# Performance work log

Hardware: AMD Instinct MI355X
Metric: run time of the kernel (lower is better)

The kernel has to match this reference:

```python
import jax, jax.numpy as jnp
from jax import lax
import numpy as np

HH = WW = 128          # backbone feature map (2048px image / stride 16)
C_IN = 512
FEAT_STRIDE = 16
N_ANCHOR = 9
NMS_THRESH = 0.7
N_PRE_NMS = 6000
N_POST_NMS = 300
MIN_SIZE = 16
NEG = jnp.float32(-1e30)


def _anchor_base(base_size=16, ratios=(0.5, 1.0, 2.0), scales=(8, 16, 32)):
    py = px = base_size / 2.0
    ab = np.zeros((len(ratios) * len(scales), 4), np.float32)
    for i, r in enumerate(ratios):
        for j, s in enumerate(scales):
            h = base_size * s * np.sqrt(r)
            w = base_size * s * np.sqrt(1.0 / r)
            ab[i * len(scales) + j] = [py - h / 2, px - w / 2, py + h / 2, px + w / 2]
    return ab


def _shifted_anchors(hh, ww):
    # (y1, x1, y2, x2) anchors enumerated row-major over (y, x), anchors innermost
    ab = _anchor_base()
    sy = np.arange(0, hh * FEAT_STRIDE, FEAT_STRIDE, dtype=np.float32)
    sx = np.arange(0, ww * FEAT_STRIDE, FEAT_STRIDE, dtype=np.float32)
    sx, sy = np.meshgrid(sx, sy)
    shift = np.stack((sy.ravel(), sx.ravel(), sy.ravel(), sx.ravel()), axis=1)
    anc = (ab[None, :, :] + shift[:, None, :]).reshape(-1, 4)
    return jnp.asarray(anc)


def _conv(x, w, b):
    y = lax.conv_general_dilated(x, w, (1, 1), 'SAME',
                                 dimension_numbers=('NHWC', 'HWIO', 'NHWC'))
    return y + b


def _loc2bbox(anchor, loc):
    sh = anchor[:, 2] - anchor[:, 0]
    sw = anchor[:, 3] - anchor[:, 1]
    scy = anchor[:, 0] + 0.5 * sh
    scx = anchor[:, 1] + 0.5 * sw
    cy = loc[:, 0] * sh + scy
    cx = loc[:, 1] * sw + scx
    h = jnp.exp(loc[:, 2]) * sh
    w = jnp.exp(loc[:, 3]) * sw
    return jnp.stack([cy - 0.5 * h, cx - 0.5 * w, cy + 0.5 * h, cx + 0.5 * w], axis=1)


def _nms(boxes, scores, thresh, n_out):
    # Greedy NMS with a fixed output size; invalid slots are zeroed.
    y1, x1, y2, x2 = boxes[:, 0], boxes[:, 1], boxes[:, 2], boxes[:, 3]
    areas = (y2 - y1) * (x2 - x1)

    def step(valid, _):
        s = jnp.where(valid, scores, NEG)
        i = jnp.argmax(s)
        ok = s[i] > NEG
        iy1 = jnp.maximum(y1, y1[i]); ix1 = jnp.maximum(x1, x1[i])
        iy2 = jnp.minimum(y2, y2[i]); ix2 = jnp.minimum(x2, x2[i])
        inter = jnp.maximum(iy2 - iy1, 0.0) * jnp.maximum(ix2 - ix1, 0.0)
        iou = inter / (areas + areas[i] - inter + 1e-9)
        valid = valid & (iou <= thresh)  # picked box suppresses itself (iou=1)
        return valid, (i, ok)

    _, (idx, oks) = lax.scan(step, jnp.ones(scores.shape, bool), None, length=n_out)
    return boxes[idx] * oks[:, None].astype(boxes.dtype)


def _proposals(loc, fg_score, anchor, img_h, img_w, scale):
    dst = _loc2bbox(anchor, loc)
    dst = jnp.stack([jnp.clip(dst[:, 0], 0.0, img_h),
                     jnp.clip(dst[:, 1], 0.0, img_w),
                     jnp.clip(dst[:, 2], 0.0, img_h),
                     jnp.clip(dst[:, 3], 0.0, img_w)], axis=1)
    min_size = MIN_SIZE * scale
    hs = dst[:, 2] - dst[:, 0]
    ws = dst[:, 3] - dst[:, 1]
    keep = (hs >= min_size) & (ws >= min_size)
    sc = jnp.where(keep, fg_score, -jnp.inf)
    top_s, top_i = lax.top_k(sc, N_PRE_NMS)
    return _nms(dst[top_i], top_s, NMS_THRESH, N_POST_NMS)


def _rpn_forward(x, conv_w, conv_b, loc_w, loc_b, score_w, score_b, img_h, img_w, scale):
    n, hh, ww, _ = x.shape
    anchor = _shifted_anchors(hh, ww)                    # [hh*ww*9, 4]
    h = jax.nn.relu(_conv(x, conv_w, conv_b))            # [n, hh, ww, 512]
    rpn_loc = _conv(h, loc_w, loc_b).reshape(n, -1, 4)   # [n, hh*ww*9, 4]
    rpn_score_map = _conv(h, score_w, score_b)           # [n, hh, ww, 18]
    soft = jax.nn.softmax(rpn_score_map.reshape(n, hh, ww, N_ANCHOR, 2), axis=-1)
    rpn_fg = soft[..., 1].reshape(n, -1)                 # [n, hh*ww*9]
    rpn_score = rpn_score_map.reshape(n, -1, 2)
    roi = _proposals(rpn_loc[0], rpn_fg[0], anchor, img_h, img_w, scale)  # [300, 4]
    return rpn_loc, rpn_score, roi, anchor


def setup_inputs() -> dict:
    key = jax.random.key(0)
    ks = jax.random.split(key, 4)
    return {
        "x": jax.random.normal(ks[0], (1, HH, WW, C_IN), jnp.float32),
        "conv_w": jax.random.normal(ks[1], (3, 3, C_IN, 512), jnp.float32) * 0.02,
        "conv_b": jnp.zeros((512,), jnp.float32),
        "loc_w": jax.random.normal(ks[2], (1, 1, 512, 36), jnp.float32) * 0.02,
        "loc_b": jnp.zeros((36,), jnp.float32),
        "score_w": jax.random.normal(ks[3], (1, 1, 512, 18), jnp.float32) * 0.02,
        "score_b": jnp.zeros((18,), jnp.float32),
        "img_h": HH * FEAT_STRIDE,
        "img_w": WW * FEAT_STRIDE,
        "scale": 1,
    }


def reference(x, conv_w, conv_b, loc_w, loc_b, score_w, score_b, img_h, img_w, scale):
    return _rpn_forward(x, conv_w, conv_b, loc_w, loc_b, score_w, score_b,
                        float(img_h), float(img_w), float(scale))
```

## Files before the change

kernel.cpp:

```cpp
#include <hip/hip_runtime.h>
#include <math.h>

typedef unsigned int u32;
typedef unsigned long long u64;
typedef _Float16 half8 __attribute__((ext_vector_type(8)));
typedef float f32x4 __attribute__((ext_vector_type(4)));

#define N_PIX 16384
#define N_ANC 147456
#define N_PRE 6000
#define TIE_BASE 6144
#define TIE_CAP  16384

#define OFF_H      0ULL
#define OFF_BOXES  33554432ULL
#define OFF_KEYS   35913728ULL
#define OFF_W54    36503552ULL
#define OFF_B54    36634624ULL
#define OFF_HIST1  36634880ULL
#define OFF_HIST2  36897024ULL
#define OFF_CTRL   37159168ULL
#define OFF_CAND   37159424ULL
#define OFF_SBOX   37339648ULL
#define OFF_MASK   37437952ULL
#define BASE_NEEDED 41961984ULL
#define OFF_XH     41961984ULL
#define OFF_XL     58739200ULL
#define OFF_WHT    75516416ULL
#define OFF_WLT    80235008ULL
#define FULL_NEEDED 84953600ULL

#define KEY_NEGINF 0x007FFFFFu

struct AB { float v[36]; };


__global__ void k_init(u32* hist1, u32* hist2, u32* ctrl, float* roi,
                       float* w54, float* b54,
                       const float* __restrict__ loc_w, const float* __restrict__ loc_b,
                       const float* __restrict__ score_w, const float* __restrict__ score_b) {
  int i = blockIdx.x * blockDim.x + threadIdx.x;
  const int stride = gridDim.x * blockDim.x;
  const int TOT = 65536 * 2 + 64 + 1200 + 32768 + 64;
  for (; i < TOT; i += stride) {
    if (i < 65536) hist1[i] = 0u;
    else if (i < 131072) hist2[i - 65536] = 0u;
    else if (i < 131136) ctrl[i - 131072] = 0u;
    else if (i < 132336) roi[i - 131136] = 0.f;
    else if (i < 165104) {
      int j = i - 132336;
      int k = j >> 6, oc = j & 63;
      float v = 0.f;
      if (oc < 36) v = loc_w[k * 36 + oc];
      else if (oc < 54) v = score_w[k * 18 + oc - 36];
      w54[(((k >> 2) << 6) + oc) * 4 + (k & 3)] = v;
    } else {
      int oc = i - 165104;
      float v = 0.f;
      if (oc < 36) v = loc_b[oc];
      else if (oc < 54) v = score_b[oc - 36];
      b54[oc] = v;
    }
  }
}

__global__ __launch_bounds__(256) void k_split_x(const float* __restrict__ x,
                                                 _Float16* __restrict__ xh,
                                                 _Float16* __restrict__ xl) {
  const int gid = blockIdx.x * blockDim.x + threadIdx.x;
  const int base = gid << 3;
  float a[8];
  *(float4*)&a[0] = *(const float4*)(x + base);
  *(float4*)&a[4] = *(const float4*)(x + base + 4);
  half8 hh, ll;
#pragma unroll
  for (int j = 0; j < 8; ++j) {
    _Float16 hi = (_Float16)a[j];
    hh[j] = hi;
    ll[j] = (_Float16)((a[j] - (float)hi) * 2048.0f);
  }
  *(half8*)(xh + base) = hh;
  *(half8*)(xl + base) = ll;
}

__global__ __launch_bounds__(256) void k_split_w(const float* __restrict__ w,
                                                 _Float16* __restrict__ whT,
                                                 _Float16* __restrict__ wlT) {
  __shared__ _Float16 th[64][72];
  __shared__ _Float16 tl[64][72];
  const int kb = blockIdx.x;
  const int cb = blockIdx.y;
  const int t  = threadIdx.x;
  {
    const int r = t >> 2, cq = t & 3;
    float a[16];
    const float* wp = w + ((size_t)(kb * 64 + r) << 9) + cb * 64 + cq * 16;
#pragma unroll
    for (int j = 0; j < 4; ++j) *(float4*)&a[j << 2] = *(const float4*)(wp + (j << 2));
    half8 h0, h1, l0, l1;
#pragma unroll
    for (int j = 0; j < 8; ++j) {
      _Float16 hi = (_Float16)a[j];
      h0[j] = hi; l0[j] = (_Float16)((a[j] - (float)hi) * 2048.0f);
    }
#pragma unroll
    for (int j = 0; j < 8; ++j) {
      _Float16 hi = (_Float16)a[8 + j];
      h1[j] = hi; l1[j] = (_Float16)((a[8 + j] - (float)hi) * 2048.0f);
    }
    *(half8*)&th[r][cq * 16]     = h0;
    *(half8*)&th[r][cq * 16 + 8] = h1;
    *(half8*)&tl[r][cq * 16]     = l0;
    *(half8*)&tl[r][cq * 16 + 8] = l1;
  }
  __syncthreads();
  {
    const int c = t >> 2, kq = t & 3;
    half8 o0, o1, p0, p1;
#pragma unroll
    for (int j = 0; j < 8; ++j) { o0[j] = th[kq * 16 + j][c];     p0[j] = tl[kq * 16 + j][c]; }
#pragma unroll
    for (int j = 0; j < 8; ++j) { o1[j] = th[kq * 16 + 8 + j][c]; p1[j] = tl[kq * 16 + 8 + j][c]; }
    const size_t dst = (size_t)(cb * 64 + c) * 4608 + kb * 64 + kq * 16;
    *(half8*)(whT + dst)     = o0;
    *(half8*)(whT + dst + 8) = o1;
    *(half8*)(wlT + dst)     = p0;
    *(half8*)(wlT + dst + 8) = p1;
  }
}

__global__ __launch_bounds__(256, 2) void k_conv_pre(const _Float16* __restrict__ xh,
                                                     const _Float16* __restrict__ xl,
                                                     const _Float16* __restrict__ whT,
                                                     const _Float16* __restrict__ wlT,
                                                     const float* __restrict__ bias,
                                                     float* __restrict__ h) {
  __shared__ _Float16 As[2][2][4][128][8];
  __shared__ _Float16 Bs[2][2][4][128][8];

  const int y  = blockIdx.x;
  const int nb = blockIdx.y;
  const int t  = threadIdx.x;
  const int wv = t >> 6, lane = t & 63;
  const int m0 = (wv >> 1) << 6;
  const int n0 = (wv & 1) << 6;
  const int fm = lane & 15;
  const int fq = lane >> 4;

  const int s_m = t >> 1;
  const int kq0 = (t & 1) << 1;
  const int ch0 = kq0 << 3;

  f32x4 acc_hh[4][4];
  f32x4 acc_x[4][4];
#pragma unroll
  for (int i = 0; i < 4; ++i)
#pragma unroll
    for (int j = 0; j < 4; ++j) { acc_hh[i][j] = (f32x4)0.f; acc_x[i][j] = (f32x4)0.f; }

  half8 rah0, rah1, ral0, ral1, rbh0, rbh1, rbl0, rbl1;

#define CONV_LOAD(KB)                                                            \
  {                                                                              \
    const int tap_  = (KB) >> 4;                                                 \
    const int ky_   = tap_ / 3, kx_ = tap_ - ky_ * 3;                            \
    const int cin0_ = ((KB) & 15) << 5;                                          \
    const int yy_ = y + ky_ - 1;                                                 \
    const int xx_ = s_m + kx_ - 1;                                               \
    if (yy_ >= 0 && yy_ < 128 && xx_ >= 0 && xx_ < 128) {                        \
      const size_t aoff_ = (((size_t)((yy_ << 7) + xx_)) << 9) + cin0_ + ch0;    \
      rah0 = *(const half8*)(xh + aoff_);                                        \
      rah1 = *(const half8*)(xh + aoff_ + 8);                                    \
      ral0 = *(const half8*)(xl + aoff_);                                        \
      ral1 = *(const half8*)(xl + aoff_ + 8);                                    \
    } else {                                                                     \
      rah0 = (half8)(_Float16)0; rah1 = (half8)(_Float16)0;                      \
      ral0 = (half8)(_Float16)0; ral1 = (half8)(_Float16)0;                      \
    }                                                                            \
    const size_t boff_ = (size_t)(nb * 128 + s_m) * 4608 + tap_ * 512 + cin0_ + ch0; \
    rbh0 = *(const half8*)(whT + boff_);                                         \
    rbh1 = *(const half8*)(whT + boff_ + 8);                                     \
    rbl0 = *(const half8*)(wlT + boff_);                                         \
    rbl1 = *(const half8*)(wlT + boff_ + 8);                                     \
  }

#define CONV_STORE(BUF)                                                          \
  {                                                                              \
    *(half8*)As[BUF][0][kq0][s_m]     = rah0;                                    \
    *(half8*)As[BUF][0][kq0 + 1][s_m] = rah1;                                    \
    *(half8*)As[BUF][1][kq0][s_m]     = ral0;                                    \
    *(half8*)As[BUF][1][kq0 + 1][s_m] = ral1;                                    \
    *(half8*)Bs[BUF][0][kq0][s_m]     = rbh0;                                    \
    *(half8*)Bs[BUF][0][kq0 + 1][s_m] = rbh1;                                    \
    *(half8*)Bs[BUF][1][kq0][s_m]     = rbl0;                                    \
    *(half8*)Bs[BUF][1][kq0 + 1][s_m] = rbl1;                                    \
  }

  CONV_LOAD(0);
  CONV_STORE(0);
  __syncthreads();

  int cur = 0;
#pragma unroll 1
  for (int kb = 0; kb < 143; ++kb) {
    half8 ah[4], al[4], bh[4], bl[4];
#pragma unroll
    for (int i = 0; i < 4; ++i) {
      ah[i] = *(const half8*)As[cur][0][fq][m0 + (i << 4) + fm];
      al[i] = *(const half8*)As[cur][1][fq][m0 + (i << 4) + fm];
      bh[i] = *(const half8*)Bs[cur][0][fq][n0 + (i << 4) + fm];
      bl[i] = *(const half8*)Bs[cur][1][fq][n0 + (i << 4) + fm];
    }
    CONV_LOAD(kb + 1);
    __builtin_amdgcn_sched_barrier(0);
    __builtin_amdgcn_s_setprio(1);
#pragma unroll
    for (int mi = 0; mi < 4; ++mi)
#pragma unroll
      for (int ni = 0; ni < 4; ++ni) {
        acc_hh[mi][ni] = __builtin_amdgcn_mfma_f32_16x16x32_f16(ah[mi], bh[ni], acc_hh[mi][ni], 0, 0, 0);
        acc_x[mi][ni]  = __builtin_amdgcn_mfma_f32_16x16x32_f16(ah[mi], bl[ni], acc_x[mi][ni], 0, 0, 0);
        acc_x[mi][ni]  = __builtin_amdgcn_mfma_f32_16x16x32_f16(al[mi], bh[ni], acc_x[mi][ni], 0, 0, 0);
      }
    __builtin_amdgcn_s_setprio(0);
    CONV_STORE(cur ^ 1);
    __syncthreads();
    cur ^= 1;
  }
  {
    half8 ah[4], al[4], bh[4], bl[4];
#pragma unroll
    for (int i = 0; i < 4; ++i) {
      ah[i] = *(const half8*)As[cur][0][fq][m0 + (i << 4) + fm];
      al[i] = *(const half8*)As[cur][1][fq][m0 + (i << 4) + fm];
      bh[i] = *(const half8*)Bs[cur][0][fq][n0 + (i << 4) + fm];
      bl[i] = *(const half8*)Bs[cur][1][fq][n0 + (i << 4) + fm];
    }
#pragma unroll
    for (int mi = 0; mi < 4; ++mi)
#pragma unroll
      for (int ni = 0; ni < 4; ++ni) {
        acc_hh[mi][ni] = __builtin_amdgcn_mfma_f32_16x16x32_f16(ah[mi], bh[ni], acc_hh[mi][ni], 0, 0, 0);
        acc_x[mi][ni]  = __builtin_amdgcn_mfma_f32_16x16x32_f16(ah[mi], bl[ni], acc_x[mi][ni], 0, 0, 0);
        acc_x[mi][ni]  = __builtin_amdgcn_mfma_f32_16x16x32_f16(al[mi], bh[ni], acc_x[mi][ni], 0, 0, 0);
      }
  }
#undef CONV_LOAD
#undef CONV_STORE

  const float inv2048 = 1.0f / 2048.0f;
#pragma unroll
  for (int mi = 0; mi < 4; ++mi)
#pragma unroll
    for (int ni = 0; ni < 4; ++ni) {
      const int col = n0 + (ni << 4) + fm;
      const float bb = bias[(nb << 7) + col];
#pragma unroll
      for (int r = 0; r < 4; ++r) {
        const int row = m0 + (mi << 4) + (fq << 2) + r;
        float v = acc_hh[mi][ni][r] + acc_x[mi][ni][r] * inv2048 + bb;
        h[(((size_t)((y << 7) + row)) << 9) + (nb << 7) + col] = fmaxf(v, 0.f);
      }
    }
}

#define APAD 40
__global__ __launch_bounds__(256, 2) void k_conv_fb(const float* __restrict__ x,
                                                    const float* __restrict__ w,
                                                    const float* __restrict__ bias,
                                                    float* __restrict__ h) {
  __shared__ _Float16 Ah[128][APAD];
  __shared__ _Float16 Al[128][APAD];
  __shared__ _Float16 Bh[128][APAD];
  __shared__ _Float16 Bl[128][APAD];

  const int y  = blockIdx.x;
  const int nb = blockIdx.y;
  const int t  = threadIdx.x;
  const int wv = t >> 6, lane = t & 63;
  const int m0 = (wv >> 1) << 6;
  const int n0 = (wv & 1) << 6;
  const int fm = lane & 15;
  const int fq = lane >> 4;
  const int sa_m = t >> 1;
  const int sa_h = (t & 1) << 4;
  const int sb_n = t & 127;
  const int sb_kg = (t >> 7) << 4;

  f32x4 acc_hh[4][4];
  f32x4 acc_x[4][4];
#pragma unroll
  for (int i = 0; i < 4; ++i)
#pragma unroll
    for (int j = 0; j < 4; ++j) { acc_hh[i][j] = (f32x4)0.f; acc_x[i][j] = (f32x4)0.f; }

#pragma unroll 1
  for (int kb = 0; kb < 144; ++kb) {
    const int tap  = kb >> 4;
    const int ky   = tap / 3, kx = tap - ky * 3;
    const int cin0 = (kb & 15) << 5;
    {
      const int yy = y + ky - 1;
      const int xx = sa_m + kx - 1;
      float av[16];
      if (yy >= 0 && yy < 128 && xx >= 0 && xx < 128) {
        const float* ap = x + (((size_t)((yy << 7) + xx)) << 9) + cin0 + sa_h;
#pragma unroll
        for (int j = 0; j < 4; ++j) *(float4*)&av[j << 2] = *(const float4*)(ap + (j << 2));
      } else {
#pragma unroll
        for (int j = 0; j < 16; ++j) av[j] = 0.f;
      }
      half8 h0, h1, l0, l1;
#pragma unroll
      for (int j = 0; j < 8; ++j) {
        _Float16 hi = (_Float16)av[j];
        h0[j] = hi; l0[j] = (_Float16)((av[j] - (float)hi) * 2048.0f);
      }
#pragma unroll
      for (int j = 0; j < 8; ++j) {
        _Float16 hi = (_Float16)av[8 + j];
        h1[j] = hi; l1[j] = (_Float16)((av[8 + j] - (float)hi) * 2048.0f);
      }
      *(half8*)&Ah[sa_m][sa_h]     = h0;
      *(half8*)&Ah[sa_m][sa_h + 8] = h1;
      *(half8*)&Al[sa_m][sa_h]     = l0;
      *(half8*)&Al[sa_m][sa_h + 8] = l1;
    }
    {
      const float* bp = w + ((size_t)(tap * 512 + cin0 + sb_kg) << 9) + (nb << 7) + sb_n;
      float bv[16];
#pragma unroll
      for (int j = 0; j < 16; ++j) bv[j] = bp[(size_t)j << 9];
      half8 h0, h1, l0, l1;
#pragma unroll
      for (int j = 0; j < 8; ++j) {
        _Float16 hi = (_Float16)bv[j];
        h0[j] = hi; l0[j] = (_Float16)((bv[j] - (float)hi) * 2048.0f);
      }
#pragma unroll
      for (int j = 0; j < 8; ++j) {
        _Float16 hi = (_Float16)bv[8 + j];
        h1[j] = hi; l1[j] = (_Float16)((bv[8 + j] - (float)hi) * 2048.0f);
      }
      *(half8*)&Bh[sb_n][sb_kg]     = h0;
      *(half8*)&Bh[sb_n][sb_kg + 8] = h1;
      *(half8*)&Bl[sb_n][sb_kg]     = l0;
      *(half8*)&Bl[sb_n][sb_kg + 8] = l1;
    }
    __syncthreads();
    half8 ah[4], al[4], bh[4], bl[4];
#pragma unroll
    for (int i = 0; i < 4; ++i) {
      ah[i] = *(const half8*)&Ah[m0 + (i << 4) + fm][fq << 3];
      al[i] = *(const half8*)&Al[m0 + (i << 4) + fm][fq << 3];
      bh[i] = *(const half8*)&Bh[n0 + (i << 4) + fm][fq << 3];
      bl[i] = *(const half8*)&Bl[n0 + (i << 4) + fm][fq << 3];
    }
#pragma unroll
    for (int mi = 0; mi < 4; ++mi)
#pragma unroll
      for (int ni = 0; ni < 4; ++ni) {
        acc_hh[mi][ni] = __builtin_amdgcn_mfma_f32_16x16x32_f16(ah[mi], bh[ni], acc_hh[mi][ni], 0, 0, 0);
        acc_x[mi][ni]  = __builtin_amdgcn_mfma_f32_16x16x32_f16(ah[mi], bl[ni], acc_x[mi][ni], 0, 0, 0);
        acc_x[mi][ni]  = __builtin_amdgcn_mfma_f32_16x16x32_f16(al[mi], bh[ni], acc_x[mi][ni], 0, 0, 0);
      }
    __syncthreads();
  }
  const float inv2048 = 1.0f / 2048.0f;
#pragma unroll
  for (int mi = 0; mi < 4; ++mi)
#pragma unroll
    for (int ni = 0; ni < 4; ++ni) {
      const int col = n0 + (ni << 4) + fm;
      const float bb = bias[(nb << 7) + col];
#pragma unroll
      for (int r = 0; r < 4; ++r) {
        const int row = m0 + (mi << 4) + (fq << 2) + r;
        float v = acc_hh[mi][ni][r] + acc_x[mi][ni][r] * inv2048 + bb;
        h[(((size_t)((y << 7) + row)) << 9) + (nb << 7) + col] = fmaxf(v, 0.f);
      }
    }
}

__global__ __launch_bounds__(256) void k_heads(const float* __restrict__ h,
        const float4* __restrict__ w54, const float* __restrict__ b54,
        float* __restrict__ out0, float* __restrict__ out1, float* __restrict__ out3,
        float4* __restrict__ boxes, u32* __restrict__ keys, u32* __restrict__ hist1,
        const int* __restrict__ p_ih, const int* __restrict__ p_iw,
        const int* __restrict__ p_sc, AB ab) {
  __shared__ float hl[16 * 512];
  __shared__ float vals[16][64];
  const int t = threadIdx.x;
  const int wv = t >> 6, lane = t & 63;
  const int pbase = blockIdx.x << 4;

#pragma unroll
  for (int j = 0; j < 8; ++j) {
    const int f = (j << 8) + t;
    ((float4*)hl)[f] = ((const float4*)(h + ((size_t)pbase << 9)))[f];
  }
  __syncthreads();

  const float* hp = hl + ((wv << 2) << 9);
  float a0 = 0.f, a1 = 0.f, a2 = 0.f, a3 = 0.f;
#pragma unroll 4
  for (int kq = 0; kq < 128; ++kq) {
    const float4 wvv = w54[(kq << 6) + lane];
    const float4 h0 = *(const float4*)(hp + (kq << 2));
    const float4 h1 = *(const float4*)(hp + 512 + (kq << 2));
    const float4 h2 = *(const float4*)(hp + 1024 + (kq << 2));
    const float4 h3 = *(const float4*)(hp + 1536 + (kq << 2));
    a0 += h0.x * wvv.x + h0.y * wvv.y + h0.z * wvv.z + h0.w * wvv.w;
    a1 += h1.x * wvv.x + h1.y * wvv.y + h1.z * wvv.z + h1.w * wvv.w;
    a2 += h2.x * wvv.x + h2.y * wvv.y + h2.z * wvv.z + h2.w * wvv.w;
    a3 += h3.x * wvv.x + h3.y * wvv.y + h3.z * wvv.z + h3.w * wvv.w;
  }
  const float bb = b54[lane];
  float av[4] = {a0 + bb, a1 + bb, a2 + bb, a3 + bb};
#pragma unroll
  for (int px = 0; px < 4; ++px) {
    const int p = pbase + (wv << 2) + px;
    vals[(wv << 2) + px][lane] = av[px];
    if (lane < 36) out0[p * 36 + lane] = av[px];
    else if (lane < 54) out1[p * 18 + lane - 36] = av[px];
  }
  __syncthreads();

  if (lane < 36) {
    const int px = lane / 9, a = lane - px * 9;
    const int p = pbase + (wv << 2) + px;
    const float* vv = vals[(wv << 2) + px];
    const float l0 = vv[(a << 2) + 0], l1 = vv[(a << 2) + 1];
    const float l2 = vv[(a << 2) + 2], l3 = vv[(a << 2) + 3];
    const float s0 = vv[36 + (a << 1)], s1 = vv[37 + (a << 1)];
    const int yq = p >> 7, xq = p & 127;
    const float fy = (float)(yq << 4), fx = (float)(xq << 4);
    const float ay1 = ab.v[(a << 2) + 0] + fy;
    const float ax1 = ab.v[(a << 2) + 1] + fx;
    const float ay2 = ab.v[(a << 2) + 2] + fy;
    const float ax2 = ab.v[(a << 2) + 3] + fx;
    const int idx = p * 9 + a;
    *(float4*)(out3 + ((size_t)idx << 2)) = make_float4(ay1, ax1, ay2, ax2);

    const float sh = ay2 - ay1, sw = ax2 - ax1;
    const float scy = ay1 + 0.5f * sh, scx = ax1 + 0.5f * sw;
    const float cy = l0 * sh + scy, cx = l1 * sw + scx;
    const float bh = expf(l2) * sh, bw = expf(l3) * sw;
    const float IH = (float)p_ih[0], IW = (float)p_iw[0];
    float d0 = fminf(fmaxf(cy - 0.5f * bh, 0.f), IH);
    float d1 = fminf(fmaxf(cx - 0.5f * bw, 0.f), IW);
    float d2 = fminf(fmaxf(cy + 0.5f * bh, 0.f), IH);
    float d3 = fminf(fmaxf(cx + 0.5f * bw, 0.f), IW);
    boxes[idx] = make_float4(d0, d1, d2, d3);

    const float minsz = 16.f * (float)p_sc[0];
    const bool keep = (d2 - d0 >= minsz) && (d3 - d1 >= minsz);
    const float mx = fmaxf(s0, s1);
    const float e0 = expf(s0 - mx), e1 = expf(s1 - mx);
    const float fg = e1 / (e0 + e1);
    const float sc = keep ? fg : -INFINITY;
    const u32 u = __float_as_uint(sc);
    const u32 key = (u & 0x80000000u) ? ~u : (u | 0x80000000u);
    keys[idx] = key;
    atomicAdd(&hist1[key >> 16], 1u);
  }
}

__global__ void k_hist2(const u32* __restrict__ keys, const u32* __restrict__ ctrl,
                        u32* __restrict__ hist2) {
  const u32 b1 = ctrl[0];
  int i = blockIdx.x * blockDim.x + threadIdx.x;
  if (i < N_ANC) {
    const u32 k = keys[i];
    if ((k >> 16) == b1) atomicAdd(&hist2[k & 0xFFFFu], 1u);
  }
}

__global__ __launch_bounds__(1024) void k_findcut(const u32* __restrict__ hist,
                                                  u32* __restrict__ ctrl, int mode) {
  __shared__ u32 csum[1024];
  __shared__ u32 suf[1024];
  const int t = threadIdx.x;
  const u32 target = (mode == 0) ? (u32)N_PRE : ((u32)N_PRE - ctrl[1]);
  const int base = t << 6;
  u32 s = 0;
  for (int i = 0; i < 64; ++i) s += hist[base + i];
  csum[t] = s;
  suf[t] = s;
  __syncthreads();
  for (int off = 1; off < 1024; off <<= 1) {
    u32 add = (t + off < 1024) ? suf[t + off] : 0u;
    __syncthreads();
    suf[t] += add;
    __syncthreads();
  }
  const u32 excl = suf[t] - csum[t];
  if (excl < target && target <= suf[t]) {
    u32 cum = excl;
    int bkt = base;
    for (int i = 63; i >= 0; --i) {
      const u32 hh = hist[base + i];
      if (cum < target && target <= cum + hh) { bkt = base + i; break; }
      cum += hh;
    }
    if (mode == 0) { ctrl[0] = (u32)bkt; ctrl[1] = cum; }
    else {
      const u32 Kstar = (ctrl[0] << 16) | (u32)bkt;
      const u32 A = ctrl[1] + cum;
      u32 need = (u32)N_PRE - A;
      if (Kstar == KEY_NEGINF) need = 0u;
      ctrl[2] = Kstar; ctrl[3] = A; ctrl[4] = need;
      ctrl[7] = A + need;
    }
  }
}

__global__ void k_compact(const u32* __restrict__ keys, u32* __restrict__ ctrl,
                          u64* __restrict__ cand) {
  const u32 Kstar = ctrl[2];
  const u32 need  = ctrl[4];
  int i = blockIdx.x * blockDim.x + threadIdx.x;
  if (i >= N_ANC) return;
  const u32 k = keys[i];
  if (k > Kstar) {
    const u32 pos = atomicAdd(&ctrl[5], 1u);
    cand[pos] = ((u64)k << 32) | (u64)(u32)(~(u32)i);
  } else if (k == Kstar && need != 0u) {
    const u32 pos = atomicAdd(&ctrl[6], 1u);
    if (pos < (u32)TIE_CAP) cand[TIE_BASE + pos] = ((u64)Kstar << 32) | (u64)(u32)(~(u32)i);
  }
}

__global__ __launch_bounds__(128) void k_rank(const u32* __restrict__ ctrl,
                                              const u64* __restrict__ cand,
                                              const float4* __restrict__ boxes,
                                              float4* __restrict__ sbox) {
  __shared__ u32 wred[2];
  const u32 A   = ctrl[3];
  const u32 tcc = min(ctrl[6], (u32)TIE_CAP);
  const u32 C   = A + tcc;
  const u32 L   = ctrl[7];
  const u32 i   = blockIdx.x;
  if (i >= C) return;
  const u64 v = (i < A) ? cand[i] : cand[TIE_BASE + (i - A)];
  const int t = threadIdx.x;
  u32 cnt = 0;
  for (u32 j = t; j < A; j += 128) cnt += (cand[j] > v);
  for (u32 j = t; j < tcc; j += 128) cnt += (cand[TIE_BASE + j] > v);
#pragma unroll
  for (int off = 32; off > 0; off >>= 1) cnt += __shfl_xor(cnt, off);
  if ((t & 63) == 0) wred[t >> 6] = cnt;
  __syncthreads();
  if (t == 0) {
    const u32 rank = wred[0] + wred[1];
    if (rank < L) {
      const u32 idx = ~((u32)(v & 0xFFFFFFFFULL));
      sbox[rank] = boxes[idx];
    }
  }
}

__global__ __launch_bounds__(64) void k_mask(const u32* __restrict__ ctrl,
                                             const float4* __restrict__ sbox,
                                             u64* __restrict__ mask) {
  const int L = (int)ctrl[7];
  const int cw = blockIdx.x;
  const int rb = blockIdx.y;
  if (cw < rb) return;
  if (rb * 64 >= L) return;
  const int lane = threadIdx.x;
  const int j = cw * 64 + lane;
  const bool jok = (j < L);
  const float4 cb = jok ? sbox[j] : make_float4(0.f, 0.f, 0.f, 0.f);
  const float careaJ = (cb.z - cb.x) * (cb.w - cb.y);
  const int rbase = rb * 64;
  const float4 rbx = (rbase + lane < L) ? sbox[rbase + lane] : make_float4(0.f, 0.f, 0.f, 0.f);
  const int rmax = min(64, L - rbase);
  for (int r = 0; r < rmax; ++r) {
    const float ry1 = __shfl(rbx.x, r), rx1 = __shfl(rbx.y, r);
    const float ry2 = __shfl(rbx.z, r), rx2 = __shfl(rbx.w, r);
    const float ra = (ry2 - ry1) * (rx2 - rx1);
    const float iy1 = fmaxf(cb.x, ry1), ix1 = fmaxf(cb.y, rx1);
    const float iy2 = fminf(cb.z, ry2), ix2 = fminf(cb.w, rx2);
    const float inter = fmaxf(iy2 - iy1, 0.f) * fmaxf(ix2 - ix1, 0.f);
    const float iou = inter / (careaJ + ra - inter + 1e-9f);
    const bool bit = jok && (iou > 0.7f);
    const u64 bal = __ballot(bit);
    if (lane == 0) mask[(size_t)(rbase + r) * 94 + cw] = bal;
  }
}

__device__ inline u64 valid_mask_fn(int base, int L) {
  const int r = L - base;
  if (r <= 0) return 0ULL;
  if (r >= 64) return ~0ULL;
  return (1ULL << r) - 1ULL;
}
__device__ inline u64 above_mask_fn(int base, int i) {
  if (i < base) return ~0ULL;
  const int s = i - base + 1;
  if (s >= 64) return 0ULL;
  return (~0ULL) << s;
}

__global__ __launch_bounds__(64) void k_greedy(const u32* __restrict__ ctrl,
                                               const float* __restrict__ sboxf,
                                               const u64* __restrict__ mask,
                                               float* __restrict__ roi) {
  const int lane = threadIdx.x;
  const int L = (int)ctrl[7];
  const int base0 = lane << 6;
  const int base1 = (64 + lane) << 6;
  const u64 v0 = valid_mask_fn(base0, L);
  const u64 v1 = (lane < 30) ? valid_mask_fn(base1, L) : 0ULL;
  u64 rem0 = 0ULL, rem1 = 0ULL;
  int i = (L > 0) ? 0 : -1;
  int kept = 0;
  while (i >= 0 && kept < 300) {
    if (lane < 4) roi[kept * 4 + lane] = sboxf[(size_t)i * 4 + lane];
    ++kept;
    rem0 |= mask[(size_t)i * 94 + lane];
    if (lane < 30) rem1 |= mask[(size_t)i * 94 + 64 + lane];
    const u64 f0 = ~rem0 & v0 & above_mask_fn(base0, i);
    const u64 f1 = ~rem1 & v1 & above_mask_fn(base1, i);
    int c0 = f0 ? (base0 + (int)__builtin_ctzll(f0)) : 0x7FFFFFFF;
    int c1 = f1 ? (base1 + (int)__builtin_ctzll(f1)) : 0x7FFFFFFF;
    int c = min(c0, c1);
#pragma unroll
    for (int off = 1; off < 64; off <<= 1) c = min(c, __shfl_xor(c, off));
    i = (c == 0x7FFFFFFF) ? -1 : c;
  }
}

extern "C" void kernel_launch(void* const* d_in, const int* in_sizes, int n_in,
                              void* d_out, int out_size, void* d_ws, size_t ws_size,
                              hipStream_t stream) {
  (void)in_sizes; (void)n_in; (void)out_size;
  if (ws_size < BASE_NEEDED) return;
  const bool fast = (ws_size >= FULL_NEEDED);

  const float* x       = (const float*)d_in[0];
  const float* conv_w  = (const float*)d_in[1];
  const float* conv_b  = (const float*)d_in[2];
  const float* loc_w   = (const float*)d_in[3];
  const float* loc_b   = (const float*)d_in[4];
  const float* score_w = (const float*)d_in[5];
  const float* score_b = (const float*)d_in[6];
  const int* p_ih = (const int*)d_in[7];
  const int* p_iw = (const int*)d_in[8];
  const int* p_sc = (const int*)d_in[9];

  float* out0 = (float*)d_out;
  float* out1 = out0 + 589824;
  float* roi  = out1 + 294912;
  float* out3 = roi + 1200;

  char* ws = (char*)d_ws;
  float*     h     = (float*)(ws + OFF_H);
  float4*    boxes = (float4*)(ws + OFF_BOXES);
  u32*       keys  = (u32*)(ws + OFF_KEYS);
  float*     w54   = (float*)(ws + OFF_W54);
  float*     b54   = (float*)(ws + OFF_B54);
  u32*       hist1 = (u32*)(ws + OFF_HIST1);
  u32*       hist2 = (u32*)(ws + OFF_HIST2);
  u32*       ctrl  = (u32*)(ws + OFF_CTRL);
  u64*       cand  = (u64*)(ws + OFF_CAND);
  float4*    sbox  = (float4*)(ws + OFF_SBOX);
  u64*       mask  = (u64*)(ws + OFF_MASK);
  _Float16*  xh    = (_Float16*)(ws + OFF_XH);
  _Float16*  xl    = (_Float16*)(ws + OFF_XL);
  _Float16*  whT   = (_Float16*)(ws + OFF_WHT);
  _Float16*  wlT   = (_Float16*)(ws + OFF_WLT);

  AB ab;
  {
    const double ratios[3] = {0.5, 1.0, 2.0};
    const double scales[3] = {8.0, 16.0, 32.0};
    for (int i = 0; i < 3; ++i)
      for (int j = 0; j < 3; ++j) {
        const double hh = 16.0 * scales[j] * sqrt(ratios[i]);
        const double wwv = 16.0 * scales[j] * sqrt(1.0 / ratios[i]);
        const int a = i * 3 + j;
        ab.v[a * 4 + 0] = (float)(8.0 - hh / 2.0);
        ab.v[a * 4 + 1] = (float)(8.0 - wwv / 2.0);
        ab.v[a * 4 + 2] = (float)(8.0 + hh / 2.0);
        ab.v[a * 4 + 3] = (float)(8.0 + wwv / 2.0);
      }
  }

  hipLaunchKernelGGL(k_init, dim3(256), dim3(256), 0, stream,
                     hist1, hist2, ctrl, roi, w54, b54, loc_w, loc_b, score_w, score_b);
  if (fast) {
    hipLaunchKernelGGL(k_split_x, dim3(4096), dim3(256), 0, stream, x, xh, xl);
    hipLaunchKernelGGL(k_split_w, dim3(72, 8), dim3(256), 0, stream, conv_w, whT, wlT);
    hipLaunchKernelGGL(k_conv_pre, dim3(128, 4), dim3(256), 0, stream, xh, xl, whT, wlT, conv_b, h);
  } else {
    hipLaunchKernelGGL(k_conv_fb, dim3(128, 4), dim3(256), 0, stream, x, conv_w, conv_b, h);
  }
  hipLaunchKernelGGL(k_heads, dim3(1024), dim3(256), 0, stream,
                     h, (const float4*)w54, b54, out0, out1, out3, boxes, keys, hist1,
                     p_ih, p_iw, p_sc, ab);
  hipLaunchKernelGGL(k_findcut, dim3(1), dim3(1024), 0, stream, hist1, ctrl, 0);
  hipLaunchKernelGGL(k_hist2, dim3(576), dim3(256), 0, stream, keys, ctrl, hist2);
  hipLaunchKernelGGL(k_findcut, dim3(1), dim3(1024), 0, stream, hist2, ctrl, 1);
  hipLaunchKernelGGL(k_compact, dim3(576), dim3(256), 0, stream, keys, ctrl, cand);
  hipLaunchKernelGGL(k_rank, dim3(TIE_BASE + TIE_CAP), dim3(128), 0, stream, ctrl, cand, boxes, sbox);
  hipLaunchKernelGGL(k_mask, dim3(94, 94), dim3(64), 0, stream, ctrl, sbox, mask);
  hipLaunchKernelGGL(k_greedy, dim3(1), dim3(64), 0, stream, ctrl, (const float*)sbox, mask, roi);
}
```

Baseline: 740.3 us.

## Use 32x32 MFMA in conv, fuse prep kernels, swizzle grid, rebalance rank/mask

The split-fp16 3x3 conv moves from 16x16x32 to 32x32x16 MFMA tiles, split into two k-substeps, with 32-bit address arithmetic and a swizzled 1-D grid for better L2 reuse of weights and input. The init, x-split and w-split kernels merge into one launch to cut launch overhead. k_rank becomes a grid-stride loop over a smaller grid, and k_mask packs four waves per block. These change register use and the scheduling of the dominant conv kernel, which could affect occupancy.

```diff
diff --git a/kernel.cpp b/kernel.cpp
--- a/kernel.cpp
+++ b/kernel.cpp
@@ -5,6 +5,7 @@
 typedef unsigned long long u64;
 typedef _Float16 half8 __attribute__((ext_vector_type(8)));
 typedef float f32x4 __attribute__((ext_vector_type(4)));
+typedef float f32x16 __attribute__((ext_vector_type(16)));
 
 #define N_PIX 16384
 #define N_ANC 147456
@@ -35,14 +36,13 @@
 struct AB { float v[36]; };
 
 
-__global__ void k_init(u32* hist1, u32* hist2, u32* ctrl, float* roi,
+__device__ __forceinline__ void d_init_body(int i0, u32* hist1, u32* hist2, u32* ctrl, float* roi,
                        float* w54, float* b54,
                        const float* __restrict__ loc_w, const float* __restrict__ loc_b,
                        const float* __restrict__ score_w, const float* __restrict__ score_b) {
-  int i = blockIdx.x * blockDim.x + threadIdx.x;
-  const int stride = gridDim.x * blockDim.x;
+  const int stride = 256 * 256;
   const int TOT = 65536 * 2 + 64 + 1200 + 32768 + 64;
-  for (; i < TOT; i += stride) {
+  for (int i = i0; i < TOT; i += stride) {
     if (i < 65536) hist1[i] = 0u;
     else if (i < 131072) hist2[i - 65536] = 0u;
     else if (i < 131136) ctrl[i - 131072] = 0u;
@@ -64,10 +64,9 @@
   }
 }
 
-__global__ __launch_bounds__(256) void k_split_x(const float* __restrict__ x,
-                                                 _Float16* __restrict__ xh,
-                                                 _Float16* __restrict__ xl) {
-  const int gid = blockIdx.x * blockDim.x + threadIdx.x;
+__device__ __forceinline__ void d_split_x_body(int b, int t, const float* __restrict__ x,
+                                               _Float16* __restrict__ xh, _Float16* __restrict__ xl) {
+  const int gid = b * 256 + t;
   const int base = gid << 3;
   float a[8];
   *(float4*)&a[0] = *(const float4*)(x + base);
@@ -83,14 +82,9 @@
   *(half8*)(xl + base) = ll;
 }
 
-__global__ __launch_bounds__(256) void k_split_w(const float* __restrict__ w,
-                                                 _Float16* __restrict__ whT,
-                                                 _Float16* __restrict__ wlT) {
-  __shared__ _Float16 th[64][72];
-  __shared__ _Float16 tl[64][72];
-  const int kb = blockIdx.x;
-  const int cb = blockIdx.y;
-  const int t  = threadIdx.x;
+__device__ __forceinline__ void d_split_w_body(int kb, int cb, int t, const float* __restrict__ w,
+                                               _Float16* __restrict__ whT, _Float16* __restrict__ wlT,
+                                               _Float16 (*th)[72], _Float16 (*tl)[72]) {
   {
     const int r = t >> 2, cq = t & 3;
     float a[16];
@@ -126,6 +120,36 @@
     *(half8*)(whT + dst + 8) = o1;
     *(half8*)(wlT + dst)     = p0;
     *(half8*)(wlT + dst + 8) = p1;
+  }
+}
+
+__global__ void k_init(u32* hist1, u32* hist2, u32* ctrl, float* roi,
+                       float* w54, float* b54,
+                       const float* __restrict__ loc_w, const float* __restrict__ loc_b,
+                       const float* __restrict__ score_w, const float* __restrict__ score_b) {
+  const int i0 = blockIdx.x * blockDim.x + threadIdx.x;
+  d_init_body(i0, hist1, hist2, ctrl, roi, w54, b54, loc_w, loc_b, score_w, score_b);
+}
+
+__global__ __launch_bounds__(256) void k_prep(const float* __restrict__ x,
+                                              _Float16* __restrict__ xh, _Float16* __restrict__ xl,
+                                              const float* __restrict__ w,
+                                              _Float16* __restrict__ whT, _Float16* __restrict__ wlT,
+                                              u32* hist1, u32* hist2, u32* ctrl, float* roi,
+                                              float* w54, float* b54,
+                                              const float* __restrict__ loc_w, const float* __restrict__ loc_b,
+                                              const float* __restrict__ score_w, const float* __restrict__ score_b) {
+  __shared__ _Float16 th[64][72];
+  __shared__ _Float16 tl[64][72];
+  const int b = blockIdx.x;
+  const int t = threadIdx.x;
+  if (b < 4096) {
+    d_split_x_body(b, t, x, xh, xl);
+  } else if (b < 4672) {
+    const int idx = b - 4096;
+    d_split_w_body(idx % 72, idx / 72, t, w, whT, wlT, th, tl);
+  } else {
+    d_init_body((b - 4672) * 256 + t, hist1, hist2, ctrl, roi, w54, b54, loc_w, loc_b, score_w, score_b);
   }
 }
 
@@ -138,25 +162,35 @@
   __shared__ _Float16 As[2][2][4][128][8];
   __shared__ _Float16 Bs[2][2][4][128][8];
 
-  const int y  = blockIdx.x;
-  const int nb = blockIdx.y;
+  const int bid = blockIdx.x;
+  const int wg  = ((bid & 7) << 6) | (bid >> 3);
+  const int nb  = wg >> 7;
+  const int y   = wg & 127;
+
   const int t  = threadIdx.x;
   const int wv = t >> 6, lane = t & 63;
   const int m0 = (wv >> 1) << 6;
   const int n0 = (wv & 1) << 6;
-  const int fm = lane & 15;
-  const int fq = lane >> 4;
+  const int ln5 = lane & 31;
+  const int kh  = lane >> 5;
 
   const int s_m = t >> 1;
   const int kq0 = (t & 1) << 1;
   const int ch0 = kq0 << 3;
 
-  f32x4 acc_hh[4][4];
-  f32x4 acc_x[4][4];
-#pragma unroll
-  for (int i = 0; i < 4; ++i)
-#pragma unroll
-    for (int j = 0; j < 4; ++j) { acc_hh[i][j] = (f32x4)0.f; acc_x[i][j] = (f32x4)0.f; }
+  f32x16 acc_hh[2][2];
+  f32x16 acc_x[2][2];
+#pragma unroll
+  for (int i = 0; i < 2; ++i)
+#pragma unroll
+    for (int j = 0; j < 2; ++j) { acc_hh[i][j] = (f32x16)0.f; acc_x[i][j] = (f32x16)0.f; }
+
+  const int ct0 = (s_m - 1) << 9;
+  const int ct1 = s_m << 9;
+  const int ct2 = (s_m + 1) << 9;
+  const bool cok0 = (s_m >= 1);
+  const bool cok2 = (s_m <= 126);
+  const u32 bb = (u32)(nb * 128 + s_m) * 4608u + (u32)ch0;
 
   half8 rah0, rah1, ral0, ral1, rbh0, rbh1, rbl0, rbl1;
 
@@ -164,11 +198,12 @@
   {                                                                              \
     const int tap_  = (KB) >> 4;                                                 \
     const int ky_   = tap_ / 3, kx_ = tap_ - ky_ * 3;                            \
-    const int cin0_ = ((KB) & 15) << 5;                                          \
-    const int yy_ = y + ky_ - 1;                                                 \
-    const int xx_ = s_m + kx_ - 1;                                               \
-    if (yy_ >= 0 && yy_ < 128 && xx_ >= 0 && xx_ < 128) {                        \
-      const size_t aoff_ = (((size_t)((yy_ << 7) + xx_)) << 9) + cin0_ + ch0;    \
+    const int yy_   = y + ky_ - 1;                                               \
+    const bool rok_ = (yy_ >= 0) && (yy_ < 128);                                 \
+    const int colterm_ = (kx_ == 0) ? ct0 : ((kx_ == 1) ? ct1 : ct2);            \
+    const bool cok_    = (kx_ == 0) ? cok0 : ((kx_ == 1) ? true : cok2);         \
+    if (rok_ && cok_) {                                                          \
+      const u32 aoff_ = (u32)((yy_ << 16) + (((KB) & 15) << 5) + ch0 + colterm_);\
       rah0 = *(const half8*)(xh + aoff_);                                        \
       rah1 = *(const half8*)(xh + aoff_ + 8);                                    \
       ral0 = *(const half8*)(xl + aoff_);                                        \
@@ -177,7 +212,7 @@
       rah0 = (half8)(_Float16)0; rah1 = (half8)(_Float16)0;                      \
       ral0 = (half8)(_Float16)0; ral1 = (half8)(_Float16)0;                      \
     }                                                                            \
-    const size_t boff_ = (size_t)(nb * 128 + s_m) * 4608 + tap_ * 512 + cin0_ + ch0; \
+    const u32 boff_ = bb + ((u32)(KB) << 5);                                     \
     rbh0 = *(const half8*)(whT + boff_);                                         \
     rbh1 = *(const half8*)(whT + boff_ + 8);                                     \
     rbl0 = *(const half8*)(wlT + boff_);                                         \
@@ -196,6 +231,30 @@
     *(half8*)Bs[BUF][1][kq0 + 1][s_m] = rbl1;                                    \
   }
 
+#define FRAGS(KS, AH, AL, BH, BL)                                                \
+  {                                                                              \
+    const int kq_ = ((KS) << 1) + kh;                                            \
+    _Pragma("unroll")                                                            \
+    for (int i = 0; i < 2; ++i) {                                                \
+      AH[i] = *(const half8*)As[cur][0][kq_][m0 + (i << 5) + ln5];               \
+      AL[i] = *(const half8*)As[cur][1][kq_][m0 + (i << 5) + ln5];               \
+      BH[i] = *(const half8*)Bs[cur][0][kq_][n0 + (i << 5) + ln5];               \
+      BL[i] = *(const half8*)Bs[cur][1][kq_][n0 + (i << 5) + ln5];               \
+    }                                                                            \
+  }
+
+#define MFMA12(AH, AL, BH, BL)                                                   \
+  {                                                                              \
+    _Pragma("unroll")                                                            \
+    for (int mi = 0; mi < 2; ++mi)                                               \
+      _Pragma("unroll")                                                          \
+      for (int ni = 0; ni < 2; ++ni) {                                           \
+        acc_hh[mi][ni] = __builtin_amdgcn_mfma_f32_32x32x16_f16(AH[mi], BH[ni], acc_hh[mi][ni], 0, 0, 0); \
+        acc_x[mi][ni]  = __builtin_amdgcn_mfma_f32_32x32x16_f16(AH[mi], BL[ni], acc_x[mi][ni], 0, 0, 0);  \
+        acc_x[mi][ni]  = __builtin_amdgcn_mfma_f32_32x32x16_f16(AL[mi], BH[ni], acc_x[mi][ni], 0, 0, 0);  \
+      }                                                                          \
+  }
+
   CONV_LOAD(0);
   CONV_STORE(0);
   __syncthreads();
@@ -203,62 +262,46 @@
   int cur = 0;
 #pragma unroll 1
   for (int kb = 0; kb < 143; ++kb) {
-    half8 ah[4], al[4], bh[4], bl[4];
-#pragma unroll
-    for (int i = 0; i < 4; ++i) {
-      ah[i] = *(const half8*)As[cur][0][fq][m0 + (i << 4) + fm];
-      al[i] = *(const half8*)As[cur][1][fq][m0 + (i << 4) + fm];
-      bh[i] = *(const half8*)Bs[cur][0][fq][n0 + (i << 4) + fm];
-      bl[i] = *(const half8*)Bs[cur][1][fq][n0 + (i << 4) + fm];
-    }
+    half8 a0h[2], a0l[2], b0h[2], b0l[2];
+    FRAGS(0, a0h, a0l, b0h, b0l);
     CONV_LOAD(kb + 1);
     __builtin_amdgcn_sched_barrier(0);
     __builtin_amdgcn_s_setprio(1);
-#pragma unroll
-    for (int mi = 0; mi < 4; ++mi)
-#pragma unroll
-      for (int ni = 0; ni < 4; ++ni) {
-        acc_hh[mi][ni] = __builtin_amdgcn_mfma_f32_16x16x32_f16(ah[mi], bh[ni], acc_hh[mi][ni], 0, 0, 0);
-        acc_x[mi][ni]  = __builtin_amdgcn_mfma_f32_16x16x32_f16(ah[mi], bl[ni], acc_x[mi][ni], 0, 0, 0);
-        acc_x[mi][ni]  = __builtin_amdgcn_mfma_f32_16x16x32_f16(al[mi], bh[ni], acc_x[mi][ni], 0, 0, 0);
-      }
+    MFMA12(a0h, a0l, b0h, b0l);
+    __builtin_amdgcn_s_setprio(0);
+    half8 a1h[2], a1l[2], b1h[2], b1l[2];
+    FRAGS(1, a1h, a1l, b1h, b1l);
+    __builtin_amdgcn_s_setprio(1);
+    MFMA12(a1h, a1l, b1h, b1l);
     __builtin_amdgcn_s_setprio(0);
     CONV_STORE(cur ^ 1);
     __syncthreads();
     cur ^= 1;
   }
   {
-    half8 ah[4], al[4], bh[4], bl[4];
-#pragma unroll
-    for (int i = 0; i < 4; ++i) {
-      ah[i] = *(const half8*)As[cur][0][fq][m0 + (i << 4) + fm];
-      al[i] = *(const half8*)As[cur][1][fq][m0 + (i << 4) + fm];
-      bh[i] = *(const half8*)Bs[cur][0][fq][n0 + (i << 4) + fm];
-      bl[i] = *(const half8*)Bs[cur][1][fq][n0 + (i << 4) + fm];
-    }
-#pragma unroll
-    for (int mi = 0; mi < 4; ++mi)
-#pragma unroll
-      for (int ni = 0; ni < 4; ++ni) {
-        acc_hh[mi][ni] = __builtin_amdgcn_mfma_f32_16x16x32_f16(ah[mi], bh[ni], acc_hh[mi][ni], 0, 0, 0);
-        acc_x[mi][ni]  = __builtin_amdgcn_mfma_f32_16x16x32_f16(ah[mi], bl[ni], acc_x[mi][ni], 0, 0, 0);
-        acc_x[mi][ni]  = __builtin_amdgcn_mfma_f32_16x16x32_f16(al[mi], bh[ni], acc_x[mi][ni], 0, 0, 0);
-      }
+    half8 a0h[2], a0l[2], b0h[2], b0l[2];
+    FRAGS(0, a0h, a0l, b0h, b0l);
+    MFMA12(a0h, a0l, b0h, b0l);
+    half8 a1h[2], a1l[2], b1h[2], b1l[2];
+    FRAGS(1, a1h, a1l, b1h, b1l);
+    MFMA12(a1h, a1l, b1h, b1l);
   }
 #undef CONV_LOAD
 #undef CONV_STORE
+#undef FRAGS
+#undef MFMA12
 
   const float inv2048 = 1.0f / 2048.0f;
 #pragma unroll
-  for (int mi = 0; mi < 4; ++mi)
-#pragma unroll
-    for (int ni = 0; ni < 4; ++ni) {
-      const int col = n0 + (ni << 4) + fm;
-      const float bb = bias[(nb << 7) + col];
-#pragma unroll
-      for (int r = 0; r < 4; ++r) {
-        const int row = m0 + (mi << 4) + (fq << 2) + r;
-        float v = acc_hh[mi][ni][r] + acc_x[mi][ni][r] * inv2048 + bb;
+  for (int mi = 0; mi < 2; ++mi)
+#pragma unroll
+    for (int ni = 0; ni < 2; ++ni) {
+      const int col = n0 + (ni << 5) + ln5;
+      const float bbv = bias[(nb << 7) + col];
+#pragma unroll
+      for (int r = 0; r < 16; ++r) {
+        const int row = m0 + (mi << 5) + (r & 3) + ((r >> 2) << 3) + (kh << 2);
+        float v = acc_hh[mi][ni][r] + acc_x[mi][ni][r] * inv2048 + bbv;
         h[(((size_t)((y << 7) + row)) << 9) + (nb << 7) + col] = fmaxf(v, 0.f);
       }
     }
@@ -541,35 +584,37 @@
   const u32 tcc = min(ctrl[6], (u32)TIE_CAP);
   const u32 C   = A + tcc;
   const u32 L   = ctrl[7];
-  const u32 i   = blockIdx.x;
-  if (i >= C) return;
-  const u64 v = (i < A) ? cand[i] : cand[TIE_BASE + (i - A)];
-  const int t = threadIdx.x;
-  u32 cnt = 0;
-  for (u32 j = t; j < A; j += 128) cnt += (cand[j] > v);
-  for (u32 j = t; j < tcc; j += 128) cnt += (cand[TIE_BASE + j] > v);
-#pragma unroll
-  for (int off = 32; off > 0; off >>= 1) cnt += __shfl_xor(cnt, off);
-  if ((t & 63) == 0) wred[t >> 6] = cnt;
-  __syncthreads();
-  if (t == 0) {
-    const u32 rank = wred[0] + wred[1];
-    if (rank < L) {
-      const u32 idx = ~((u32)(v & 0xFFFFFFFFULL));
-      sbox[rank] = boxes[idx];
-    }
-  }
-}
-
-__global__ __launch_bounds__(64) void k_mask(const u32* __restrict__ ctrl,
-                                             const float4* __restrict__ sbox,
-                                             u64* __restrict__ mask) {
+  const int t   = threadIdx.x;
+  for (u32 i = blockIdx.x; i < C; i += gridDim.x) {
+    const u64 v = (i < A) ? cand[i] : cand[TIE_BASE + (i - A)];
+    u32 cnt = 0;
+    for (u32 j = t; j < A; j += 128) cnt += (cand[j] > v);
+    for (u32 j = t; j < tcc; j += 128) cnt += (cand[TIE_BASE + j] > v);
+#pragma unroll
+    for (int off = 32; off > 0; off >>= 1) cnt += __shfl_xor(cnt, off);
+    if ((t & 63) == 0) wred[t >> 6] = cnt;
+    __syncthreads();
+    if (t == 0) {
+      const u32 rank = wred[0] + wred[1];
+      if (rank < L) {
+        const u32 idx = ~((u32)(v & 0xFFFFFFFFULL));
+        sbox[rank] = boxes[idx];
+      }
+    }
+    __syncthreads();
+  }
+}
+
+__global__ __launch_bounds__(256) void k_mask(const u32* __restrict__ ctrl,
+                                              const float4* __restrict__ sbox,
+                                              u64* __restrict__ mask) {
   const int L = (int)ctrl[7];
-  const int cw = blockIdx.x;
   const int rb = blockIdx.y;
-  if (cw < rb) return;
   if (rb * 64 >= L) return;
-  const int lane = threadIdx.x;
+  const int wv = threadIdx.x >> 6;
+  const int lane = threadIdx.x & 63;
+  const int cw = (blockIdx.x << 2) + wv;
+  if (cw > 93 || cw < rb) return;
   const int j = cw * 64 + lane;
   const bool jok = (j < L);
   const float4 cb = jok ? sbox[j] : make_float4(0.f, 0.f, 0.f, 0.f);
@@ -689,13 +734,14 @@
       }
   }
 
-  hipLaunchKernelGGL(k_init, dim3(256), dim3(256), 0, stream,
-                     hist1, hist2, ctrl, roi, w54, b54, loc_w, loc_b, score_w, score_b);
   if (fast) {
-    hipLaunchKernelGGL(k_split_x, dim3(4096), dim3(256), 0, stream, x, xh, xl);
-    hipLaunchKernelGGL(k_split_w, dim3(72, 8), dim3(256), 0, stream, conv_w, whT, wlT);
-    hipLaunchKernelGGL(k_conv_pre, dim3(128, 4), dim3(256), 0, stream, xh, xl, whT, wlT, conv_b, h);
+    hipLaunchKernelGGL(k_prep, dim3(4928), dim3(256), 0, stream,
+                       x, xh, xl, conv_w, whT, wlT,
+                       hist1, hist2, ctrl, roi, w54, b54, loc_w, loc_b, score_w, score_b);
+    hipLaunchKernelGGL(k_conv_pre, dim3(512), dim3(256), 0, stream, xh, xl, whT, wlT, conv_b, h);
   } else {
+    hipLaunchKernelGGL(k_init, dim3(256), dim3(256), 0, stream,
+                       hist1, hist2, ctrl, roi, w54, b54, loc_w, loc_b, score_w, score_b);
     hipLaunchKernelGGL(k_conv_fb, dim3(128, 4), dim3(256), 0, stream, x, conv_w, conv_b, h);
   }
   hipLaunchKernelGGL(k_heads, dim3(1024), dim3(256), 0, stream,
@@ -705,7 +751,7 @@
   hipLaunchKernelGGL(k_hist2, dim3(576), dim3(256), 0, stream, keys, ctrl, hist2);
   hipLaunchKernelGGL(k_findcut, dim3(1), dim3(1024), 0, stream, hist2, ctrl, 1);
   hipLaunchKernelGGL(k_compact, dim3(576), dim3(256), 0, stream, keys, ctrl, cand);
-  hipLaunchKernelGGL(k_rank, dim3(TIE_BASE + TIE_CAP), dim3(128), 0, stream, ctrl, cand, boxes, sbox);
-  hipLaunchKernelGGL(k_mask, dim3(94, 94), dim3(64), 0, stream, ctrl, sbox, mask);
+  hipLaunchKernelGGL(k_rank, dim3(8192), dim3(128), 0, stream, ctrl, cand, boxes, sbox);
+  hipLaunchKernelGGL(k_mask, dim3(24, 94), dim3(256), 0, stream, ctrl, sbox, mask);
   hipLaunchKernelGGL(k_greedy, dim3(1), dim3(64), 0, stream, ctrl, (const float*)sbox, mask, roi);
 }
```

Measured after the change: 776.6 us. 4.9% more time.
